# Performance work log

Hardware: AMD Instinct MI355X
Metric: run time of the kernel (lower is better)

The kernel has to match this reference:

```python
import jax, jax.numpy as jnp
import numpy as np
from jax import lax

WINDOW_SIZE = 11
SIGMA = 1.5
DATA_RANGE = 1.0


def _gaussian_window(channels):
    coords = jnp.arange(WINDOW_SIZE, dtype=jnp.float32) - WINDOW_SIZE // 2
    g = jnp.exp(-coords ** 2 / (2.0 * SIGMA ** 2))
    g = g / g.sum()
    w2d = jnp.outer(g, g)
    w2d = w2d / w2d.sum()
    # depthwise kernel: (C, 1, K, K) in OIHW with feature_group_count=C
    return jnp.broadcast_to(w2d, (channels, 1, WINDOW_SIZE, WINDOW_SIZE))


def _dwconv(x, window, channels):
    pad = WINDOW_SIZE // 2
    return lax.conv_general_dilated(
        x, window,
        window_strides=(1, 1),
        padding=[(pad, pad), (pad, pad)],
        dimension_numbers=('NCHW', 'OIHW', 'NCHW'),
        feature_group_count=channels,
    )


def setup_inputs() -> dict:
    key = jax.random.key(0)
    k1, k2 = jax.random.split(key)
    B, C, H, W = 16, 3, 512, 512
    x = jax.random.uniform(k1, (B, C, H, W), dtype=jnp.float32)
    y = jax.random.uniform(k2, (B, C, H, W), dtype=jnp.float32)
    return {"x": x, "y": y}


def reference(x, y):
    channels = x.shape[1]
    window = _gaussian_window(channels)
    mu_x = _dwconv(x, window, channels)
    mu_y = _dwconv(y, window, channels)
    mu_x2 = mu_x * mu_x
    mu_y2 = mu_y * mu_y
    mu_xy = mu_x * mu_y
    sigma_x2 = _dwconv(x * x, window, channels) - mu_x2
    sigma_y2 = _dwconv(y * y, window, channels) - mu_y2
    sigma_xy = _dwconv(x * y, window, channels) - mu_xy
    c1 = (0.01 * DATA_RANGE) ** 2
    c2 = (0.03 * DATA_RANGE) ** 2
    ssim_map = (2 * mu_xy + c1) * (2 * sigma_xy + c2) / (
        (mu_x2 + mu_y2 + c1) * (sigma_x2 + sigma_y2 + c2) + 1e-08)
    per_image = ssim_map.mean(axis=(1, 2, 3))
    return 1.0 - per_image.mean()
```

## Files before the change

### kernel.cpp

```cpp
#include <hip/hip_runtime.h>
#include <math.h>


#define IMG_W 512
#define IMG_H 512
#define PLANES 48
#define TX 64
#define TY 32
#define RAD 5
#define KW 11
#define NPAIR 21
#define SJ 65
#define NT 256
#define GDX (IMG_W / TX)
#define GDY (IMG_H / TY)
#define NBLK (GDX * GDY * PLANES)

typedef _Float16 h2 __attribute__((ext_vector_type(2)));

#if __has_builtin(__builtin_amdgcn_fdot2)
__device__ __forceinline__ float DOT2(h2 a, h2 b, float c) {
    return __builtin_amdgcn_fdot2(a, b, c, false);
}
#else
__device__ __forceinline__ float DOT2(h2 a, h2 b, float c) {
    return c + (float)a.x * (float)b.x + (float)a.y * (float)b.y;
}
#endif

__device__ __forceinline__ h2 pkrtz(float a, float b) {
    auto t = __builtin_amdgcn_cvt_pkrtz(a, b);
    h2 r;
    __builtin_memcpy(&r, &t, sizeof(r));
    return r;
}

template<bool INTERIOR>
__device__ __forceinline__ void hpass_item(
    int r, int g, int ty0, int bx0,
    const float* __restrict__ xp, const float* __restrict__ yp,
    _Float16* __restrict__ hbh,
    const h2 (* __restrict__ w2)[6])
{
    const int gy = ty0 + r;
    const int j0 = bx0 + g * 8;
    const float4 z4 = make_float4(0.f, 0.f, 0.f, 0.f);

    h2 sh[11], dh[11];
    {
        const bool rowok = INTERIOR || ((unsigned)gy < (unsigned)IMG_H);
        const float* rowx = xp + (size_t)gy * IMG_W;
        const float* rowy = yp + (size_t)gy * IMG_W;
        #pragma unroll
        for (int v = 0; v < 6; ++v) {
            const int gx = j0 - 8 + 4 * v;
            float4 xa, ya;
            if (rowok && (INTERIOR || ((unsigned)gx < (unsigned)IMG_W))) {
                xa = *(const float4*)(rowx + gx);
                ya = *(const float4*)(rowy + gx);
            } else { xa = z4; ya = z4; }
            if (2*v >= 1 && 2*v <= 10) {
                const h2 xh = pkrtz(xa.x, xa.y), yh = pkrtz(ya.x, ya.y);
                sh[2*v] = xh + yh;
                dh[2*v] = xh - yh;
            }
            if (2*v + 1 <= 10) {
                const h2 xh = pkrtz(xa.z, xa.w), yh = pkrtz(ya.z, ya.w);
                sh[2*v+1] = xh + yh;
                dh[2*v+1] = xh - yh;
            }
        }
    }

    const int pp = r >> 1, rr = r & 1;
    _Float16* base = hbh + ((pp * 4) * SJ + g * 8) * 2 + rr;
    const int pstr = SJ * 2;

    #pragma unroll
    for (int u = 0; u < 8; ++u) {
        const int t0 = (u + 3) >> 1;
        const h2* wt = w2[(u & 1) ^ 1];
        float fS = 0.f, fD = 0.f;
        #pragma unroll
        for (int q = 0; q < 6; ++q) {
            fS = DOT2(sh[t0 + q], wt[q], fS);
            fD = DOT2(dh[t0 + q], wt[q], fD);
        }
        base[2*u + 0*pstr] = (_Float16)fS;
        base[2*u + 1*pstr] = (_Float16)fD;
    }

    h2 s2h[11], d2h[11];
    #pragma unroll
    for (int t = 1; t <= 10; ++t) {
        s2h[t] = sh[t] * sh[t];
        d2h[t] = dh[t] * dh[t];
    }

    #pragma unroll
    for (int u = 0; u < 8; ++u) {
        const int t0 = (u + 3) >> 1;
        const h2* wt = w2[(u & 1) ^ 1];
        float fS2 = 0.f, fD2 = 0.f;
        #pragma unroll
        for (int q = 0; q < 6; ++q) {
            fS2 = DOT2(s2h[t0 + q], wt[q], fS2);
            fD2 = DOT2(d2h[t0 + q], wt[q], fD2);
        }
        base[2*u + 2*pstr] = (_Float16)fS2;
        base[2*u + 3*pstr] = (_Float16)fD2;
    }
}

__global__ __launch_bounds__(NT, 5) void ssim_tile_kernel(
    const float* __restrict__ x, const float* __restrict__ y,
    float* __restrict__ partials)
{
    __shared__ h2 hb[NPAIR][4][SJ];
    __shared__ float wave_sums[NT / 64];

    float w[KW];
    {
        float s = 0.f;
        #pragma unroll
        for (int k = 0; k < KW; ++k) {
            const float d = (float)(k - RAD);
            w[k] = expf(-d * d * (1.f / (2.f * 1.5f * 1.5f)));
            s += w[k];
        }
        const float inv = 1.f / s;
        #pragma unroll
        for (int k = 0; k < KW; ++k) w[k] *= inv;
    }
    _Float16 wh[KW];
    float cv;
    {
        float s2 = 0.f;
        #pragma unroll
        for (int k = 0; k < KW; ++k) { wh[k] = (_Float16)w[k]; s2 += (float)wh[k]; }
        cv = 1.f / (s2 * s2);
    }
    h2 w2[2][6];
    #pragma unroll
    for (int q = 0; q < 5; ++q) { w2[0][q].x = wh[2*q];   w2[0][q].y = wh[2*q+1]; }
    w2[0][5].x = wh[10]; w2[0][5].y = (_Float16)0.f;
    w2[1][0].x = (_Float16)0.f; w2[1][0].y = wh[0];
    #pragma unroll
    for (int q = 1; q < 6; ++q) { w2[1][q].x = wh[2*q-1]; w2[1][q].y = wh[2*q]; }

    const int tid = threadIdx.x;
    const int plane = blockIdx.z;
    const float* __restrict__ xp = x + (size_t)plane * IMG_H * IMG_W;
    const float* __restrict__ yp = y + (size_t)plane * IMG_H * IMG_W;
    const int bx0 = blockIdx.x * TX;
    const int ty0 = blockIdx.y * TY - RAD;

    const bool interior =
        (bx0 >= 8) && (bx0 + TX + 8 <= IMG_W) &&
        (ty0 >= 0) && (ty0 + 2 * NPAIR <= IMG_H);

    _Float16* hbh = (_Float16*)hb;

    if (interior) {
        hpass_item<true>(tid >> 3, tid & 7, ty0, bx0, xp, yp, hbh, w2);
        if (tid < 42 * 8 - NT)
            hpass_item<true>(32 + (tid >> 3), tid & 7, ty0, bx0, xp, yp, hbh, w2);
    } else {
        hpass_item<false>(tid >> 3, tid & 7, ty0, bx0, xp, yp, hbh, w2);
        if (tid < 42 * 8 - NT)
            hpass_item<false>(32 + (tid >> 3), tid & 7, ty0, bx0, xp, yp, hbh, w2);
    }
    __syncthreads();

    const int j  = tid & 63;
    const int P0 = (tid >> 6) * 4;

    float acc[4][8];
    #pragma unroll
    for (int p = 0; p < 4; ++p)
        #pragma unroll
        for (int u = 0; u < 8; ++u) acc[p][u] = 0.f;

    #pragma unroll
    for (int pp = 0; pp < 9; ++pp) {
        h2 v[4];
        #pragma unroll
        for (int p = 0; p < 4; ++p)
            v[p] = hb[P0 + pp][p][j];
        const int ulo = (2 * pp - 10) > 0 ? (2 * pp - 10) : 0;
        const int uhi = (2 * pp + 1) < 7 ? (2 * pp + 1) : 7;
        #pragma unroll
        for (int u = ulo; u <= uhi; ++u) {
            const h2 wv = w2[u & 1][pp - (u >> 1)];
            #pragma unroll
            for (int p = 0; p < 4; ++p)
                acc[p][u] = DOT2(v[p], wv, acc[p][u]);
        }
    }

    float local = 0.f;
    #pragma unroll
    for (int u = 0; u < 8; ++u) {
        const float mS = acc[0][u] * cv, mD = acc[1][u] * cv;
        const float eS = acc[2][u] * cv, eD = acc[3][u] * cv;
        const float ms2 = mS * mS, md2 = mD * mD;
        const float Pm = 0.5f * (ms2 - md2);
        const float Qm = 0.5f * (ms2 + md2);
        const float Pe = 0.5f * (eS - eD);
        const float Qe = 0.5f * (eS + eD);
        const float c1 = 1e-4f, c2 = 9e-4f;
        const float num = (Pm + c1) * (Pe - Pm + c2);
        const float den = (Qm + c1) * (Qe - Qm + c2) + 1e-8f;
        local += num * __builtin_amdgcn_rcpf(den);
    }

    #pragma unroll
    for (int off = 32; off > 0; off >>= 1)
        local += __shfl_down(local, off, 64);
    const int lane = tid & 63, wv = tid >> 6;
    if (lane == 0) wave_sums[wv] = local;
    __syncthreads();
    if (tid == 0) {
        const float s = wave_sums[0] + wave_sums[1] + wave_sums[2] + wave_sums[3];
        const int bid = blockIdx.x + GDX * (blockIdx.y + GDY * blockIdx.z);
        partials[bid] = s;
    }
}

__global__ __launch_bounds__(NT) void ssim_finalize_kernel(
    const float* __restrict__ partials, float* __restrict__ out)
{
    const int tid = threadIdx.x;
    double s = 0.0;
    #pragma unroll 4
    for (int i = tid; i < NBLK; i += NT) s += (double)partials[i];
    #pragma unroll
    for (int off = 32; off > 0; off >>= 1)
        s += __shfl_down(s, off, 64);
    __shared__ double ws_[NT / 64];
    const int lane = tid & 63, wv = tid >> 6;
    if (lane == 0) ws_[wv] = s;
    __syncthreads();
    if (tid == 0) {
        const double t = ws_[0] + ws_[1] + ws_[2] + ws_[3];
        const double n = (double)PLANES * IMG_H * IMG_W;
        out[0] = (float)(1.0 - t / n);
    }
}

extern "C" void kernel_launch(void* const* d_in, const int* in_sizes, int n_in,
                              void* d_out, int out_size, void* d_ws, size_t ws_size,
                              hipStream_t stream)
{
    const float* x = (const float*)d_in[0];
    const float* y = (const float*)d_in[1];
    float* out = (float*)d_out;
    float* partials = (float*)d_ws;

    dim3 grid(GDX, GDY, PLANES);
    ssim_tile_kernel<<<grid, NT, 0, stream>>>(x, y, partials);
    ssim_finalize_kernel<<<1, NT, 0, stream>>>(partials, out);
}
```

Before: 143.5 us.

## Compute separable Gaussian passes with MFMA banded-matrix multiplies

Replaces the packed fdot2 horizontal and vertical convolution passes with 16x16x32 f16 MFMA instructions that multiply input tiles by banded Toeplitz weight matrices built per lane. The input tile is first staged in LDS as half-precision sum/difference planes. Horizontal results go into a transposed LDS buffer so the vertical pass can also be done as an MFMA. This moves the convolution work onto the matrix cores but adds more LDS traffic, an extra barrier, and lower occupancy (launch bounds drop from 5 to 3).

```diff
diff --git a/kernel.cpp b/kernel.cpp
--- a/kernel.cpp
+++ b/kernel.cpp
@@ -8,25 +8,21 @@
 #define TX 64
 #define TY 32
 #define RAD 5
-#define KW 11
-#define NPAIR 21
-#define SJ 65
 #define NT 256
 #define GDX (IMG_W / TX)
 #define GDY (IMG_H / TY)
 #define NBLK (GDX * GDY * PLANES)
 
+#define SROWS 48
+#define SCH   20
+#define SSTR  88
+#define HSTR  56
+#define GC    (1.f / (2.f * 1.5f * 1.5f))
+
 typedef _Float16 h2 __attribute__((ext_vector_type(2)));
-
-#if __has_builtin(__builtin_amdgcn_fdot2)
-__device__ __forceinline__ float DOT2(h2 a, h2 b, float c) {
-    return __builtin_amdgcn_fdot2(a, b, c, false);
-}
-#else
-__device__ __forceinline__ float DOT2(h2 a, h2 b, float c) {
-    return c + (float)a.x * (float)b.x + (float)a.y * (float)b.y;
-}
-#endif
+typedef _Float16 h4 __attribute__((ext_vector_type(4)));
+typedef _Float16 h8 __attribute__((ext_vector_type(8)));
+typedef float f32x4 __attribute__((ext_vector_type(4)));
 
 __device__ __forceinline__ h2 pkrtz(float a, float b) {
     auto t = __builtin_amdgcn_cvt_pkrtz(a, b);
@@ -35,190 +31,145 @@
     return r;
 }
 
-template<bool INTERIOR>
-__device__ __forceinline__ void hpass_item(
-    int r, int g, int ty0, int bx0,
-    const float* __restrict__ xp, const float* __restrict__ yp,
-    _Float16* __restrict__ hbh,
-    const h2 (* __restrict__ w2)[6])
-{
-    const int gy = ty0 + r;
-    const int j0 = bx0 + g * 8;
-    const float4 z4 = make_float4(0.f, 0.f, 0.f, 0.f);
-
-    h2 sh[11], dh[11];
-    {
-        const bool rowok = INTERIOR || ((unsigned)gy < (unsigned)IMG_H);
-        const float* rowx = xp + (size_t)gy * IMG_W;
-        const float* rowy = yp + (size_t)gy * IMG_W;
-        #pragma unroll
-        for (int v = 0; v < 6; ++v) {
-            const int gx = j0 - 8 + 4 * v;
-            float4 xa, ya;
-            if (rowok && (INTERIOR || ((unsigned)gx < (unsigned)IMG_W))) {
-                xa = *(const float4*)(rowx + gx);
-                ya = *(const float4*)(rowy + gx);
-            } else { xa = z4; ya = z4; }
-            if (2*v >= 1 && 2*v <= 10) {
-                const h2 xh = pkrtz(xa.x, xa.y), yh = pkrtz(ya.x, ya.y);
-                sh[2*v] = xh + yh;
-                dh[2*v] = xh - yh;
-            }
-            if (2*v + 1 <= 10) {
-                const h2 xh = pkrtz(xa.z, xa.w), yh = pkrtz(ya.z, ya.w);
-                sh[2*v+1] = xh + yh;
-                dh[2*v+1] = xh - yh;
-            }
-        }
-    }
-
-    const int pp = r >> 1, rr = r & 1;
-    _Float16* base = hbh + ((pp * 4) * SJ + g * 8) * 2 + rr;
-    const int pstr = SJ * 2;
-
-    #pragma unroll
-    for (int u = 0; u < 8; ++u) {
-        const int t0 = (u + 3) >> 1;
-        const h2* wt = w2[(u & 1) ^ 1];
-        float fS = 0.f, fD = 0.f;
-        #pragma unroll
-        for (int q = 0; q < 6; ++q) {
-            fS = DOT2(sh[t0 + q], wt[q], fS);
-            fD = DOT2(dh[t0 + q], wt[q], fD);
-        }
-        base[2*u + 0*pstr] = (_Float16)fS;
-        base[2*u + 1*pstr] = (_Float16)fD;
-    }
-
-    h2 s2h[11], d2h[11];
-    #pragma unroll
-    for (int t = 1; t <= 10; ++t) {
-        s2h[t] = sh[t] * sh[t];
-        d2h[t] = dh[t] * dh[t];
-    }
-
-    #pragma unroll
-    for (int u = 0; u < 8; ++u) {
-        const int t0 = (u + 3) >> 1;
-        const h2* wt = w2[(u & 1) ^ 1];
-        float fS2 = 0.f, fD2 = 0.f;
-        #pragma unroll
-        for (int q = 0; q < 6; ++q) {
-            fS2 = DOT2(s2h[t0 + q], wt[q], fS2);
-            fD2 = DOT2(d2h[t0 + q], wt[q], fD2);
-        }
-        base[2*u + 2*pstr] = (_Float16)fS2;
-        base[2*u + 3*pstr] = (_Float16)fD2;
-    }
-}
-
-__global__ __launch_bounds__(NT, 5) void ssim_tile_kernel(
+__device__ __forceinline__ h4 pack4(f32x4 a) {
+    const h2 lo = pkrtz(a[0], a[1]), hi = pkrtz(a[2], a[3]);
+    h4 v;
+    v[0] = lo.x; v[1] = lo.y; v[2] = hi.x; v[3] = hi.y;
+    return v;
+}
+
+__global__ __launch_bounds__(NT, 3) void ssim_tile_kernel(
     const float* __restrict__ x, const float* __restrict__ y,
     float* __restrict__ partials)
 {
-    __shared__ h2 hb[NPAIR][4][SJ];
+    __shared__ __align__(16) _Float16 sIn[SROWS * SSTR];
+    __shared__ __align__(16) _Float16 dIn[SROWS * SSTR];
+    __shared__ __align__(16) _Float16 Ht[4 * TX * HSTR];
     __shared__ float wave_sums[NT / 64];
 
-    float w[KW];
+    const int tid = threadIdx.x;
+    const int l   = tid & 63, wid = tid >> 6;
+    const int q   = l >> 4,  fc  = l & 15;
+
+    float inv, cv;
     {
         float s = 0.f;
         #pragma unroll
-        for (int k = 0; k < KW; ++k) {
+        for (int k = 0; k < 11; ++k) {
             const float d = (float)(k - RAD);
-            w[k] = expf(-d * d * (1.f / (2.f * 1.5f * 1.5f)));
-            s += w[k];
-        }
-        const float inv = 1.f / s;
-        #pragma unroll
-        for (int k = 0; k < KW; ++k) w[k] *= inv;
-    }
-    _Float16 wh[KW];
-    float cv;
-    {
+            s += expf(-d * d * GC);
+        }
+        inv = 1.f / s;
         float s2 = 0.f;
         #pragma unroll
-        for (int k = 0; k < KW; ++k) { wh[k] = (_Float16)w[k]; s2 += (float)wh[k]; }
+        for (int k = 0; k < 11; ++k) {
+            const float d = (float)(k - RAD);
+            s2 += (float)(_Float16)(expf(-d * d * GC) * inv);
+        }
         cv = 1.f / (s2 * s2);
     }
-    h2 w2[2][6];
-    #pragma unroll
-    for (int q = 0; q < 5; ++q) { w2[0][q].x = wh[2*q];   w2[0][q].y = wh[2*q+1]; }
-    w2[0][5].x = wh[10]; w2[0][5].y = (_Float16)0.f;
-    w2[1][0].x = (_Float16)0.f; w2[1][0].y = wh[0];
-    #pragma unroll
-    for (int q = 1; q < 6; ++q) { w2[1][q].x = wh[2*q-1]; w2[1][q].y = wh[2*q]; }
-
-    const int tid = threadIdx.x;
+
+    h8 whB, wvA;
+    #pragma unroll
+    for (int e = 0; e < 8; ++e) {
+        const int t  = 8 * q + e;
+        const int k1 = t - fc - 3;
+        const int k2 = t - fc;
+        float g1 = 0.f, g2 = 0.f;
+        if (k1 >= 0 && k1 <= 10) {
+            const float d = (float)(k1 - RAD);
+            g1 = expf(-d * d * GC) * inv;
+        }
+        if (k2 >= 0 && k2 <= 10) {
+            const float d = (float)(k2 - RAD);
+            g2 = expf(-d * d * GC) * inv;
+        }
+        whB[e] = (_Float16)g1;
+        wvA[e] = (_Float16)g2;
+    }
+
     const int plane = blockIdx.z;
     const float* __restrict__ xp = x + (size_t)plane * IMG_H * IMG_W;
     const float* __restrict__ yp = y + (size_t)plane * IMG_H * IMG_W;
-    const int bx0 = blockIdx.x * TX;
-    const int ty0 = blockIdx.y * TY - RAD;
-
-    const bool interior =
-        (bx0 >= 8) && (bx0 + TX + 8 <= IMG_W) &&
-        (ty0 >= 0) && (ty0 + 2 * NPAIR <= IMG_H);
-
-    _Float16* hbh = (_Float16*)hb;
-
-    if (interior) {
-        hpass_item<true>(tid >> 3, tid & 7, ty0, bx0, xp, yp, hbh, w2);
-        if (tid < 42 * 8 - NT)
-            hpass_item<true>(32 + (tid >> 3), tid & 7, ty0, bx0, xp, yp, hbh, w2);
-    } else {
-        hpass_item<false>(tid >> 3, tid & 7, ty0, bx0, xp, yp, hbh, w2);
-        if (tid < 42 * 8 - NT)
-            hpass_item<false>(32 + (tid >> 3), tid & 7, ty0, bx0, xp, yp, hbh, w2);
-    }
-    __syncthreads();
-
-    const int j  = tid & 63;
-    const int P0 = (tid >> 6) * 4;
-
-    float acc[4][8];
-    #pragma unroll
-    for (int p = 0; p < 4; ++p)
+    const int C0 = blockIdx.x * TX;
+    const int R0 = blockIdx.y * TY;
+
+    for (int it = tid; it < SROWS * SCH; it += NT) {
+        const int i  = it / SCH;
+        const int c  = it - i * SCH;
+        const int gr = R0 - RAD + i;
+        const int gc = C0 - 8 + 4 * c;
+        float4 xa = make_float4(0.f, 0.f, 0.f, 0.f);
+        float4 ya = make_float4(0.f, 0.f, 0.f, 0.f);
+        if ((unsigned)gr < (unsigned)IMG_H && (unsigned)gc < (unsigned)IMG_W) {
+            xa = *(const float4*)(xp + (size_t)gr * IMG_W + gc);
+            ya = *(const float4*)(yp + (size_t)gr * IMG_W + gc);
+        }
+        const h2 x01 = pkrtz(xa.x, xa.y), x23 = pkrtz(xa.z, xa.w);
+        const h2 y01 = pkrtz(ya.x, ya.y), y23 = pkrtz(ya.z, ya.w);
+        const h2 s01 = x01 + y01, s23 = x23 + y23;
+        const h2 d01 = x01 - y01, d23 = x23 - y23;
+        h4 sv, dv;
+        sv[0] = s01.x; sv[1] = s01.y; sv[2] = s23.x; sv[3] = s23.y;
+        dv[0] = d01.x; dv[1] = d01.y; dv[2] = d23.x; dv[3] = d23.y;
+        *(h4*)&sIn[i * SSTR + 4 * c] = sv;
+        *(h4*)&dIn[i * SSTR + 4 * c] = dv;
+    }
+    __syncthreads();
+
+    const int c0 = 16 * wid;
+    const f32x4 zz = {0.f, 0.f, 0.f, 0.f};
+    #pragma unroll
+    for (int i0 = 0; i0 < SROWS; i0 += 16) {
+        const int aoff = (i0 + fc) * SSTR + c0 + 8 * q;
+        const h8 sA = *(const h8*)&sIn[aoff];
+        const h8 dA = *(const h8*)&dIn[aoff];
+        const h8 s2A = sA * sA;
+        const h8 d2A = dA * dA;
+        const f32x4 hS  = __builtin_amdgcn_mfma_f32_16x16x32_f16(sA,  whB, zz, 0, 0, 0);
+        const f32x4 hD  = __builtin_amdgcn_mfma_f32_16x16x32_f16(dA,  whB, zz, 0, 0, 0);
+        const f32x4 hS2 = __builtin_amdgcn_mfma_f32_16x16x32_f16(s2A, whB, zz, 0, 0, 0);
+        const f32x4 hD2 = __builtin_amdgcn_mfma_f32_16x16x32_f16(d2A, whB, zz, 0, 0, 0);
+        const int hoff = (c0 + fc) * HSTR + i0 + 4 * q;
+        *(h4*)&Ht[0 * TX * HSTR + hoff] = pack4(hS);
+        *(h4*)&Ht[1 * TX * HSTR + hoff] = pack4(hD);
+        *(h4*)&Ht[2 * TX * HSTR + hoff] = pack4(hS2);
+        *(h4*)&Ht[3 * TX * HSTR + hoff] = pack4(hD2);
+    }
+    __syncthreads();
+
+    float local = 0.f;
+    #pragma unroll
+    for (int m = 0; m < TY / 16; ++m) {
+        const int boff = (c0 + fc) * HSTR + 16 * m + 8 * q;
+        const f32x4 aS  = __builtin_amdgcn_mfma_f32_16x16x32_f16(
+            wvA, *(const h8*)&Ht[0 * TX * HSTR + boff], zz, 0, 0, 0);
+        const f32x4 aD  = __builtin_amdgcn_mfma_f32_16x16x32_f16(
+            wvA, *(const h8*)&Ht[1 * TX * HSTR + boff], zz, 0, 0, 0);
+        const f32x4 aS2 = __builtin_amdgcn_mfma_f32_16x16x32_f16(
+            wvA, *(const h8*)&Ht[2 * TX * HSTR + boff], zz, 0, 0, 0);
+        const f32x4 aD2 = __builtin_amdgcn_mfma_f32_16x16x32_f16(
+            wvA, *(const h8*)&Ht[3 * TX * HSTR + boff], zz, 0, 0, 0);
         #pragma unroll
-        for (int u = 0; u < 8; ++u) acc[p][u] = 0.f;
-
-    #pragma unroll
-    for (int pp = 0; pp < 9; ++pp) {
-        h2 v[4];
-        #pragma unroll
-        for (int p = 0; p < 4; ++p)
-            v[p] = hb[P0 + pp][p][j];
-        const int ulo = (2 * pp - 10) > 0 ? (2 * pp - 10) : 0;
-        const int uhi = (2 * pp + 1) < 7 ? (2 * pp + 1) : 7;
-        #pragma unroll
-        for (int u = ulo; u <= uhi; ++u) {
-            const h2 wv = w2[u & 1][pp - (u >> 1)];
-            #pragma unroll
-            for (int p = 0; p < 4; ++p)
-                acc[p][u] = DOT2(v[p], wv, acc[p][u]);
-        }
-    }
-
-    float local = 0.f;
-    #pragma unroll
-    for (int u = 0; u < 8; ++u) {
-        const float mS = acc[0][u] * cv, mD = acc[1][u] * cv;
-        const float eS = acc[2][u] * cv, eD = acc[3][u] * cv;
-        const float ms2 = mS * mS, md2 = mD * mD;
-        const float Pm = 0.5f * (ms2 - md2);
-        const float Qm = 0.5f * (ms2 + md2);
-        const float Pe = 0.5f * (eS - eD);
-        const float Qe = 0.5f * (eS + eD);
-        const float c1 = 1e-4f, c2 = 9e-4f;
-        const float num = (Pm + c1) * (Pe - Pm + c2);
-        const float den = (Qm + c1) * (Qe - Qm + c2) + 1e-8f;
-        local += num * __builtin_amdgcn_rcpf(den);
+        for (int r = 0; r < 4; ++r) {
+            const float mS = aS[r]  * cv, mD = aD[r]  * cv;
+            const float eS = aS2[r] * cv, eD = aD2[r] * cv;
+            const float ms2 = mS * mS, md2 = mD * mD;
+            const float Pm = 0.5f * (ms2 - md2);
+            const float Qm = 0.5f * (ms2 + md2);
+            const float Pe = 0.5f * (eS - eD);
+            const float Qe = 0.5f * (eS + eD);
+            const float c1 = 1e-4f, c2 = 9e-4f;
+            const float num = (Pm + c1) * (Pe - Pm + c2);
+            const float den = (Qm + c1) * (Qe - Qm + c2) + 1e-8f;
+            local += num * __builtin_amdgcn_rcpf(den);
+        }
     }
 
     #pragma unroll
     for (int off = 32; off > 0; off >>= 1)
         local += __shfl_down(local, off, 64);
-    const int lane = tid & 63, wv = tid >> 6;
-    if (lane == 0) wave_sums[wv] = local;
+    if (l == 0) wave_sums[wid] = local;
     __syncthreads();
     if (tid == 0) {
         const float s = wave_sums[0] + wave_sums[1] + wave_sums[2] + wave_sums[3];
```

Measured after the change: 148.5 us. 3.5% more time.
